# Performance work log

Measured on AMD Instinct MI355X. Metric: run time of the kernel, lower is better.

The kernel has to match this reference:

```python
import jax, jax.numpy as jnp
import numpy as np


def setup_inputs() -> dict:
    key = jax.random.key(0)
    k1, k2 = jax.random.split(key)
    B, N, M, D = 4, 8192, 8192, 3
    prediction = jax.random.normal(k1, (B, N, D), dtype=jnp.float32)
    ground_truth = jax.random.normal(k2, (B, M, D), dtype=jnp.float32)
    return {"prediction": prediction, "ground_truth": ground_truth}


def reference(prediction, ground_truth):
    # Pairwise Euclidean distances via the expansion trick (avoids the
    x2 = jnp.sum(prediction * prediction, axis=-1)          # [B, N]
    y2 = jnp.sum(ground_truth * ground_truth, axis=-1)      # [B, M]
    xy = jnp.einsum('bnd,bmd->bnm', prediction, ground_truth)  # [B, N, M]
    d = jnp.sqrt(jnp.maximum(x2[..., :, None] + y2[..., None, :] - 2.0 * xy, 0.0))
    # Directed Hausdorff distances, then symmetric max.
    d_xy = jnp.max(jnp.min(d, axis=-1), axis=-1)  # max_n min_m  -> [B]
    d_yx = jnp.max(jnp.min(d, axis=-2), axis=-1)  # max_m min_n  -> [B]
    return jnp.maximum(d_xy, d_yx)
```

## Files before the change

### kernel.cpp

```cpp
#include <hip/hip_runtime.h>
#include <math.h>

#define BATCH 4
#define NPTS 8192
#define TB 256
#define NB 2
#define XW (NB * 32)
#define XSPAN (4 * XW)
#define XBLKS (NPTS / XSPAN)
#define YSPAN 1024
#define YBLKS (NPTS / YSPAN)
#define YTILES (YSPAN / 32)

typedef _Float16 f16x8 __attribute__((ext_vector_type(8)));
typedef float f32x16 __attribute__((ext_vector_type(16)));


__device__ __forceinline__ float tree17(f32x16 d, float r) {
    float v0 = fminf(fminf(d[0], d[1]), d[2]);
    float v1 = fminf(fminf(d[3], d[4]), d[5]);
    float v2 = fminf(fminf(d[6], d[7]), d[8]);
    float v3 = fminf(fminf(d[9], d[10]), d[11]);
    float v4 = fminf(fminf(d[12], d[13]), d[14]);
    float w0 = fminf(fminf(v0, v1), v2);
    float w1 = fminf(fminf(v3, v4), d[15]);
    return fminf(fminf(w0, w1), r);
}

__global__ __launch_bounds__(TB) void hd_mfma(const float* __restrict__ pred,
                                              const float* __restrict__ gt,
                                              unsigned* __restrict__ minbits) {
    const int tid = threadIdx.x;
    const int xblk = blockIdx.x % XBLKS;
    const int yblk = blockIdx.x / XBLKS;
    const int b = blockIdx.y;
    const int dir = blockIdx.z;

    const float* X = (dir == 0) ? pred + (size_t)b * NPTS * 3 : gt + (size_t)b * NPTS * 3;
    const float* Y = (dir == 0) ? gt + (size_t)b * NPTS * 3 : pred + (size_t)b * NPTS * 3;

    __shared__ __align__(16) _Float16 As[YSPAN * 16];

    const int ybase = yblk * YSPAN;
    for (int p = tid; p < YSPAN; p += TB) {
        int gp = ybase + p;
        float y0 = Y[3 * gp], y1 = Y[3 * gp + 1], y2 = Y[3 * gp + 2];
        _Float16 h0 = (_Float16)y0, h1 = (_Float16)y1, h2 = (_Float16)y2;
        _Float16 l0 = (_Float16)(y0 - (float)h0);
        _Float16 l1 = (_Float16)(y1 - (float)h1);
        _Float16 l2 = (_Float16)(y2 - (float)h2);
        float ys = fmaf(y0, y0, fmaf(y1, y1, y2 * y2));
        _Float16 sh = (_Float16)ys, sl = (_Float16)(ys - (float)sh);
        const _Float16 n2 = (_Float16)(-2.f);
        _Float16 A0 = n2 * h0, A1 = n2 * h1, A2 = n2 * h2;
        _Float16 C0 = n2 * l0, C1 = n2 * l1, C2 = n2 * l2;
        f16x8 g0 = {A0, A1, A2, A0, A1, A2, C0, C1};
        f16x8 g1 = {C2, C0, C1, C2, sh, sl, (_Float16)1.f, (_Float16)1.f};
        *(f16x8*)&As[p * 16] = g0;
        *(f16x8*)&As[p * 16 + 8] = g1;
    }

    const int wave = tid >> 6, lane = tid & 63, half = lane >> 5, ln = lane & 31;
    const int xw = xblk * XSPAN + wave * XW;
    f16x8 bf[NB];
#pragma unroll
    for (int i = 0; i < NB; ++i) {
        int px = xw + i * 32 + ln;
        float x0 = X[3 * px], x1 = X[3 * px + 1], x2 = X[3 * px + 2];
        _Float16 h0 = (_Float16)x0, h1 = (_Float16)x1, h2 = (_Float16)x2;
        _Float16 l0 = (_Float16)(x0 - (float)h0);
        _Float16 l1 = (_Float16)(x1 - (float)h1);
        _Float16 l2 = (_Float16)(x2 - (float)h2);
        float xs = fmaf(x0, x0, fmaf(x1, x1, x2 * x2));
        _Float16 sh = (_Float16)xs, sl = (_Float16)(xs - (float)sh);
        f16x8 g0 = {h0, h1, h2, l0, l1, l2, h0, h1};
        f16x8 g1 = {h2, l0, l1, l2, (_Float16)1.f, (_Float16)1.f, sh, sl};
        bf[i] = half ? g1 : g0;
    }
    __syncthreads();

    const f32x16 zc = {0.f, 0.f, 0.f, 0.f, 0.f, 0.f, 0.f, 0.f,
                       0.f, 0.f, 0.f, 0.f, 0.f, 0.f, 0.f, 0.f};
    float rmin[NB];
#pragma unroll
    for (int i = 0; i < NB; ++i) rmin[i] = 3.0e38f;

    int aoff = ln * 16 + half * 8;
    for (int u = 0; u < YTILES; ++u) {
        f16x8 af = *(f16x8*)&As[aoff];
        aoff += 512;
#pragma unroll
        for (int i = 0; i < NB; ++i) {
            f32x16 d = __builtin_amdgcn_mfma_f32_32x32x16_f16(af, bf[i], zc, 0, 0, 0);
            rmin[i] = tree17(d, rmin[i]);
        }
    }

    unsigned* mb = minbits + ((size_t)(dir * BATCH + b)) * NPTS;
#pragma unroll
    for (int i = 0; i < NB; ++i) {
        float v = fminf(rmin[i], __shfl_xor(rmin[i], 32, 64));
        if (lane < 32) {
            v = fmaxf(v, 0.f);
            atomicMin(&mb[xw + i * 32 + ln], __float_as_uint(v));
        }
    }
}

__global__ __launch_bounds__(256) void hd_reduce(const unsigned* __restrict__ minbits,
                                                 float* __restrict__ out) {
    const int tid = threadIdx.x;
    const int b = blockIdx.x;
    const uint4* p0 = (const uint4*)(minbits + (size_t)b * NPTS);
    const uint4* p1 = (const uint4*)(minbits + (size_t)(BATCH + b) * NPTS);
    unsigned vmax = 0u;
    for (int i = tid; i < NPTS / 4; i += 256) {
        uint4 u = p0[i];
        uint4 v = p1[i];
        unsigned a = max(max(u.x, u.y), max(u.z, u.w));
        unsigned c = max(max(v.x, v.y), max(v.z, v.w));
        vmax = max(vmax, max(a, c));
    }
    __shared__ unsigned sm[256];
    sm[tid] = vmax;
    __syncthreads();
    for (int s = 128; s > 0; s >>= 1) {
        if (tid < s) sm[tid] = max(sm[tid], sm[tid + s]);
        __syncthreads();
    }
    if (tid == 0) out[b] = sqrtf(__uint_as_float(sm[0]));
}

extern "C" void kernel_launch(void* const* d_in, const int* in_sizes, int n_in,
                              void* d_out, int out_size, void* d_ws, size_t ws_size,
                              hipStream_t stream) {
    const float* pred = (const float*)d_in[0];
    const float* gt = (const float*)d_in[1];
    unsigned* minbits = (unsigned*)d_ws;

    (void)hipMemsetAsync(minbits, 0xFF, (size_t)2 * BATCH * NPTS * sizeof(unsigned),
                         stream);
    hd_mfma<<<dim3(XBLKS * YBLKS, BATCH, 2), TB, 0, stream>>>(pred, gt, minbits);
    hd_reduce<<<BATCH, 256, 0, stream>>>(minbits, (float*)d_out);
}
```

Measured before the change: 85.10 us.

## Fuse final max-reduction into MFMA kernel and hand-schedule paired MFMAs

Removes the separate reduction kernel. A global counter, initialised by the same memset, elects the last finishing block, and that block reduces the per-point minima with wave shuffles and writes the outputs. The inner loop now issues the two MFMAs per A fragment through inline assembly and prefetches the next LDS fragment, to overlap LDS loads with matrix work. The intent is to save a kernel launch and tighten the MFMA issue. The risks are that inline asm hides MFMA result hazards from the compiler, and that the memory fence comes after the counter increment rather than before it.

Result: slower. 90.85 us (+6.8%).

```diff
diff --git a/kernel.cpp b/kernel.cpp
--- a/kernel.cpp
+++ b/kernel.cpp
@@ -11,6 +11,7 @@
 #define YSPAN 1024
 #define YBLKS (NPTS / YSPAN)
 #define YTILES (YSPAN / 32)
+#define NBLK (XBLKS * YBLKS * BATCH * 2)
 
 typedef _Float16 f16x8 __attribute__((ext_vector_type(8)));
 typedef float f32x16 __attribute__((ext_vector_type(16)));
@@ -27,9 +28,20 @@
     return fminf(fminf(w0, w1), r);
 }
 
+#define MFMA2(D0, D1, AF)                                                     \
+    asm volatile(                                                             \
+        "s_nop 1\n\t"                                                         \
+        "v_mfma_f32_32x32x16_f16 %0, %2, %3, %5\n\t"                          \
+        "v_mfma_f32_32x32x16_f16 %1, %2, %4, %5\n\t"                          \
+        "s_nop 1\n\t"                                                         \
+        : "=&v"(D0), "=&v"(D1)                                                \
+        : "v"(AF), "v"(bf0), "v"(bf1), "v"(zc));
+
 __global__ __launch_bounds__(TB) void hd_mfma(const float* __restrict__ pred,
                                               const float* __restrict__ gt,
-                                              unsigned* __restrict__ minbits) {
+                                              unsigned* __restrict__ minbits,
+                                              unsigned* __restrict__ counter,
+                                              float* __restrict__ out) {
     const int tid = threadIdx.x;
     const int xblk = blockIdx.x % XBLKS;
     const int yblk = blockIdx.x / XBLKS;
@@ -62,7 +74,7 @@
 
     const int wave = tid >> 6, lane = tid & 63, half = lane >> 5, ln = lane & 31;
     const int xw = xblk * XSPAN + wave * XW;
-    f16x8 bf[NB];
+    f16x8 bf0, bf1;
 #pragma unroll
     for (int i = 0; i < NB; ++i) {
         int px = xw + i * 32 + ln;
@@ -75,60 +87,66 @@
         _Float16 sh = (_Float16)xs, sl = (_Float16)(xs - (float)sh);
         f16x8 g0 = {h0, h1, h2, l0, l1, l2, h0, h1};
         f16x8 g1 = {h2, l0, l1, l2, (_Float16)1.f, (_Float16)1.f, sh, sl};
-        bf[i] = half ? g1 : g0;
+        if (i == 0) bf0 = half ? g1 : g0;
+        else        bf1 = half ? g1 : g0;
     }
     __syncthreads();
 
     const f32x16 zc = {0.f, 0.f, 0.f, 0.f, 0.f, 0.f, 0.f, 0.f,
                        0.f, 0.f, 0.f, 0.f, 0.f, 0.f, 0.f, 0.f};
-    float rmin[NB];
-#pragma unroll
-    for (int i = 0; i < NB; ++i) rmin[i] = 3.0e38f;
+    float rmin0 = 3.0e38f, rmin1 = 3.0e38f;
 
-    int aoff = ln * 16 + half * 8;
-    for (int u = 0; u < YTILES; ++u) {
-        f16x8 af = *(f16x8*)&As[aoff];
-        aoff += 512;
-#pragma unroll
-        for (int i = 0; i < NB; ++i) {
-            f32x16 d = __builtin_amdgcn_mfma_f32_32x32x16_f16(af, bf[i], zc, 0, 0, 0);
-            rmin[i] = tree17(d, rmin[i]);
-        }
+    const int base = ln * 16 + half * 8;
+    f16x8 afa = *(const f16x8*)&As[base];
+    for (int u = 0; u < YTILES; u += 2) {
+        f16x8 afb = *(const f16x8*)&As[base + (u + 1) * 512];
+        f32x16 d0, d1, d2, d3;
+        MFMA2(d0, d1, afa)
+        rmin0 = tree17(d0, rmin0);
+        rmin1 = tree17(d1, rmin1);
+        afa = *(const f16x8*)&As[base + (((u + 2) & (YTILES - 1)) * 512)];
+        MFMA2(d2, d3, afb)
+        rmin0 = tree17(d2, rmin0);
+        rmin1 = tree17(d3, rmin1);
     }
 
     unsigned* mb = minbits + ((size_t)(dir * BATCH + b)) * NPTS;
-#pragma unroll
-    for (int i = 0; i < NB; ++i) {
-        float v = fminf(rmin[i], __shfl_xor(rmin[i], 32, 64));
-        if (lane < 32) {
-            v = fmaxf(v, 0.f);
-            atomicMin(&mb[xw + i * 32 + ln], __float_as_uint(v));
-        }
+    {
+        float v = fminf(rmin0, __shfl_xor(rmin0, 32, 64));
+        if (lane < 32) atomicMin(&mb[xw + ln], __float_as_uint(fmaxf(v, 0.f)));
     }
-}
+    {
+        float v = fminf(rmin1, __shfl_xor(rmin1, 32, 64));
+        if (lane < 32) atomicMin(&mb[xw + 32 + ln], __float_as_uint(fmaxf(v, 0.f)));
+    }
 
-__global__ __launch_bounds__(256) void hd_reduce(const unsigned* __restrict__ minbits,
-                                                 float* __restrict__ out) {
-    const int tid = threadIdx.x;
-    const int b = blockIdx.x;
-    const uint4* p0 = (const uint4*)(minbits + (size_t)b * NPTS);
-    const uint4* p1 = (const uint4*)(minbits + (size_t)(BATCH + b) * NPTS);
+    __syncthreads();
+    __shared__ int is_last;
+    if (tid == 0) {
+        unsigned old = atomicAdd(counter, 1u);
+        is_last = (old == (unsigned)(NBLK - 2));
+    }
+    __syncthreads();
+    if (!is_last) return;
+    __threadfence();
+
+    const uint4* q0 = (const uint4*)(minbits + (size_t)wave * NPTS);
+    const uint4* q1 = (const uint4*)(minbits + (size_t)(BATCH + wave) * NPTS);
     unsigned vmax = 0u;
-    for (int i = tid; i < NPTS / 4; i += 256) {
-        uint4 u = p0[i];
-        uint4 v = p1[i];
+#pragma unroll 4
+    for (int j = 0; j < NPTS / 4 / 64; ++j) {
+        uint4 u = q0[lane + 64 * j];
+        uint4 v = q1[lane + 64 * j];
         unsigned a = max(max(u.x, u.y), max(u.z, u.w));
         unsigned c = max(max(v.x, v.y), max(v.z, v.w));
         vmax = max(vmax, max(a, c));
     }
-    __shared__ unsigned sm[256];
-    sm[tid] = vmax;
-    __syncthreads();
-    for (int s = 128; s > 0; s >>= 1) {
-        if (tid < s) sm[tid] = max(sm[tid], sm[tid + s]);
-        __syncthreads();
+#pragma unroll
+    for (int off = 32; off > 0; off >>= 1) {
+        unsigned o = (unsigned)__shfl_down((int)vmax, off, 64);
+        vmax = max(vmax, o);
     }
-    if (tid == 0) out[b] = sqrtf(__uint_as_float(sm[0]));
+    if (lane == 0) out[wave] = sqrtf(__uint_as_float(vmax));
 }
 
 extern "C" void kernel_launch(void* const* d_in, const int* in_sizes, int n_in,
@@ -137,9 +155,10 @@
     const float* pred = (const float*)d_in[0];
     const float* gt = (const float*)d_in[1];
     unsigned* minbits = (unsigned*)d_ws;
+    unsigned* counter = minbits + 2 * BATCH * NPTS;
 
-    (void)hipMemsetAsync(minbits, 0xFF, (size_t)2 * BATCH * NPTS * sizeof(unsigned),
-                         stream);
-    hd_mfma<<<dim3(XBLKS * YBLKS, BATCH, 2), TB, 0, stream>>>(pred, gt, minbits);
-    hd_reduce<<<BATCH, 256, 0, stream>>>(minbits, (float*)d_out);
+    (void)hipMemsetAsync(minbits, 0xFF,
+                         ((size_t)2 * BATCH * NPTS + 1) * sizeof(unsigned), stream);
+    hd_mfma<<<dim3(XBLKS * YBLKS, BATCH, 2), TB, 0, stream>>>(pred, gt, minbits, counter,
+                                                              (float*)d_out);
 }
```
